# Kernel tuning notes

Measured on AMD Instinct MI355X. Metric: run time of the kernel, lower is better.

The kernel has to match this reference:

```python
import jax, jax.numpy as jnp
import numpy as np

D_MODEL = 2048
N_HEADS = 16
HEAD_DIM = D_MODEL // N_HEADS  # 128
MAX_SEQ = 2048
ROPE_BASE = 10000.0


def _rope(t, start_pos):
    # t: (B, S, Hn, head_dim); standard interleaved-pair RoPE
    B, S, Hn, hd = t.shape
    inv_freq = 1.0 / (ROPE_BASE ** (jnp.arange(0, hd, 2, dtype=jnp.float32) / hd))  # (hd/2,)
    pos = jnp.arange(start_pos, start_pos + S, dtype=jnp.float32)                    # (S,)
    ang = pos[:, None] * inv_freq[None, :]                                           # (S, hd/2)
    cos = jnp.cos(ang)[None, :, None, :]
    sin = jnp.sin(ang)[None, :, None, :]
    x1 = t[..., 0::2]
    x2 = t[..., 1::2]
    o1 = x1 * cos - x2 * sin
    o2 = x1 * sin + x2 * cos
    return jnp.stack([o1, o2], axis=-1).reshape(t.shape)


def setup_inputs() -> dict:
    key = jax.random.key(0)
    ks = jax.random.split(key, 9)
    s = 1.0 / np.sqrt(D_MODEL)
    return {
        "x": jax.random.normal(ks[0], (4, 2048, D_MODEL), dtype=jnp.float32),
        "wq": jax.random.uniform(ks[1], (D_MODEL, D_MODEL), jnp.float32, -s, s),
        "bq": jax.random.uniform(ks[2], (D_MODEL,), jnp.float32, -s, s),
        "wk": jax.random.uniform(ks[3], (D_MODEL, HEAD_DIM), jnp.float32, -s, s),
        "bk": jax.random.uniform(ks[4], (HEAD_DIM,), jnp.float32, -s, s),
        "wv": jax.random.uniform(ks[5], (D_MODEL, HEAD_DIM), jnp.float32, -s, s),
        "bv": jax.random.uniform(ks[6], (HEAD_DIM,), jnp.float32, -s, s),
        "wo": jax.random.uniform(ks[7], (D_MODEL, D_MODEL), jnp.float32, -s, s),
        "bo": jax.random.uniform(ks[8], (D_MODEL,), jnp.float32, -s, s),
    }


def reference(x, wq, bq, wk, bk, wv, bv, wo, bo):
    # Prefill path: start_pos=0, kv_cache=None.
    B, S, D = x.shape
    q = (x @ wq + bq).reshape(B, S, N_HEADS, HEAD_DIM)  # (B,S,H,hd)
    k = (x @ wk + bk).reshape(B, S, 1, HEAD_DIM)        # (B,S,1,hd) shared KV head
    v = (x @ wv + bv).reshape(B, S, 1, HEAD_DIM)
    q = _rope(q, 0)
    k = _rope(k, 0)
    qh = q.transpose(0, 2, 1, 3)          # (B,H,S,hd)
    kh = k.transpose(0, 2, 1, 3)          # (B,1,S,hd)  -> kv_cache entry
    vh = v.transpose(0, 2, 1, 3)
    scores = jnp.einsum("bhqd,bkd->bhqk", qh, kh[:, 0]) / jnp.sqrt(
        jnp.asarray(HEAD_DIM, dtype=x.dtype))
    # original buffer: tril(ones) with zeros replaced by -inf -> allowed positions get +1
    tril = jnp.tril(jnp.ones((S, S), dtype=bool))
    mask = jnp.where(tril, jnp.asarray(1.0, x.dtype), jnp.asarray(-jnp.inf, x.dtype))
    scores = scores + mask[None, None, :, :]
    p = jax.nn.softmax(scores, axis=-1)                 # (B,H,S,S)
    attn = jnp.einsum("bhqk,bkd->bhqd", p, vh[:, 0])    # (B,H,S,hd)
    out = attn.transpose(0, 2, 1, 3).reshape(B, S, D) @ wo + bo
    return (out, kh, vh)
```

## Files before the change

kernel.cpp:

```cpp
#include <hip/hip_runtime.h>
#include <hip/hip_bf16.h>
#include <cstdint>
#include <cstddef>

#define SEQ 2048
#define DM 2048
#define NHEADS 16
#define HD 128
#define NTOK 8192
#define BATCH 4

typedef __bf16 bf16_t;
typedef bf16_t bf16x8 __attribute__((ext_vector_type(8)));
typedef float f32x4 __attribute__((ext_vector_type(4)));

__device__ __forceinline__ void async_copy16(const bf16_t* g, bf16_t* l) {
  __builtin_amdgcn_global_load_lds(
      (const __attribute__((address_space(1))) unsigned int*)g,
      (__attribute__((address_space(3))) unsigned int*)l, 16, 0, 0);
}

__device__ __forceinline__ void store_out(float* p, float v)  { *p = v; }
__device__ __forceinline__ void store_out(bf16_t* p, float v) { *p = (bf16_t)v; }


__global__ void convert_x_bf16(const float* __restrict__ in, bf16_t* __restrict__ out, int n4) {
  int i = blockIdx.x * 256 + threadIdx.x;
  if (i >= n4) return;
  float4 v = ((const float4*)in)[i];
  union { ushort4 u; bf16_t b[4]; } o;
  o.b[0] = (bf16_t)v.x; o.b[1] = (bf16_t)v.y; o.b[2] = (bf16_t)v.z; o.b[3] = (bf16_t)v.w;
  *(ushort4*)(out + (size_t)i * 4) = o.u;
}

__global__ void transpose_f32_to_bf16(const float* __restrict__ in, bf16_t* __restrict__ out,
                                      int R, int C) {
  __shared__ float tile[32][33];
  int c0 = blockIdx.x * 32, r0 = blockIdx.y * 32;
  int tx = threadIdx.x & 31, ty = threadIdx.x >> 5;
  for (int i = ty; i < 32; i += 8) tile[i][tx] = in[(size_t)(r0 + i) * C + c0 + tx];
  __syncthreads();
  for (int i = ty; i < 32; i += 8) out[(size_t)(c0 + i) * R + r0 + tx] = (bf16_t)tile[tx][i];
}

template <typename OutT>
__global__ __launch_bounds__(256) void gemm_bt(const bf16_t* __restrict__ A,
                                               const bf16_t* __restrict__ Bt,
                                               const float* __restrict__ bias,
                                               OutT* __restrict__ C, int M, int N, int K) {
  __shared__ bf16_t As[128 * 32];
  __shared__ bf16_t Bs[128 * 32];
  const int tid = threadIdx.x;
  const int lane = tid & 63;
  const int wv = tid >> 6;
  const int wi = wv >> 1, wj = wv & 1;
  const int quad = lane >> 4, l16 = lane & 15;
  const size_t m0 = (size_t)blockIdx.x * 128, n0 = (size_t)blockIdx.y * 128;

  f32x4 acc[4][4] = {};

  const bf16_t* ag = A + (m0 + (tid >> 2)) * K + (tid & 3) * 8;
  const bf16_t* bg = Bt + (n0 + (tid >> 2)) * K + (tid & 3) * 8;
  bf16_t* asd = As + tid * 8;
  bf16_t* bsd = Bs + tid * 8;
  const int nk = K >> 5;
  for (int kt = 0; kt < nk; kt++) {
    async_copy16(ag, asd);
    async_copy16(ag + (size_t)64 * K, asd + 64 * 32);
    async_copy16(bg, bsd);
    async_copy16(bg + (size_t)64 * K, bsd + 64 * 32);
    ag += 32; bg += 32;
    __syncthreads();
    bf16x8 af[4], bf[4];
#pragma unroll
    for (int mt = 0; mt < 4; mt++)
      af[mt] = *(const bf16x8*)(As + (wi * 64 + mt * 16 + l16) * 32 + quad * 8);
#pragma unroll
    for (int nt = 0; nt < 4; nt++)
      bf[nt] = *(const bf16x8*)(Bs + (wj * 64 + nt * 16 + l16) * 32 + quad * 8);
#pragma unroll
    for (int mt = 0; mt < 4; mt++)
#pragma unroll
      for (int nt = 0; nt < 4; nt++)
        acc[mt][nt] = __builtin_amdgcn_mfma_f32_16x16x32_bf16(af[mt], bf[nt], acc[mt][nt], 0, 0, 0);
    __syncthreads();
  }
#pragma unroll
  for (int nt = 0; nt < 4; nt++) {
    float bb = bias[n0 + wj * 64 + nt * 16 + l16];
#pragma unroll
    for (int mt = 0; mt < 4; mt++) {
      size_t row = m0 + wi * 64 + mt * 16 + quad * 4;
      size_t col = n0 + wj * 64 + nt * 16 + l16;
#pragma unroll
      for (int r = 0; r < 4; r++) store_out(&C[(row + r) * N + col], acc[mt][nt][r] + bb);
    }
  }
}

#define ROPE_C 0.14391156831212787f
#define ATT_SCALE 0.1275174462517703f

__global__ void rope_q_kernel(bf16_t* __restrict__ q) {
  int idx = blockIdx.x * 256 + threadIdx.x;
  int tok = idx >> 8;
  int c0 = (idx & 255) * 8;
  int s = tok & (SEQ - 1);
  int d0 = c0 & (HD - 1);
  union { uint4 u; ushort us[8]; } v;
  v.u = *(const uint4*)(q + (size_t)tok * DM + c0);
  float x[8];
#pragma unroll
  for (int j = 0; j < 8; j++) x[j] = __uint_as_float((uint32_t)v.us[j] << 16);
#pragma unroll
  for (int j = 0; j < 4; j++) {
    int i = (d0 >> 1) + j;
    float fr = __expf(-(float)i * ROPE_C);
    float ang = (float)s * fr;
    float sn, cs; __sincosf(ang, &sn, &cs);
    float o1 = (x[2 * j] * cs - x[2 * j + 1] * sn) * ATT_SCALE;
    float o2 = (x[2 * j] * sn + x[2 * j + 1] * cs) * ATT_SCALE;
    x[2 * j] = o1; x[2 * j + 1] = o2;
  }
  union { uint4 u; ushort us[8]; } w;
#pragma unroll
  for (int j = 0; j < 8; j++) {
    union { float f; uint32_t u; } t; t.f = x[j];
    uint32_t r = (t.u + 0x7fff + ((t.u >> 16) & 1)) >> 16;
    w.us[j] = (ushort)r;
  }
  *(uint4*)(q + (size_t)tok * DM + c0) = w.u;
}

__global__ void rope_kv_kernel(const float* __restrict__ kvf, float* __restrict__ kh,
                               float* __restrict__ vh, bf16_t* __restrict__ kbf) {
  int idx = blockIdx.x * 256 + threadIdx.x;
  int t = idx >> 6;
  int i = idx & 63;
  int s = t & (SEQ - 1);
  const float* base = kvf + (size_t)t * 256;
  float x1 = base[2 * i], x2 = base[2 * i + 1];
  float fr = __expf(-(float)i * ROPE_C);
  float ang = (float)s * fr;
  float sn, cs; __sincosf(ang, &sn, &cs);
  float k1 = x1 * cs - x2 * sn, k2 = x1 * sn + x2 * cs;
  size_t o = (size_t)t * HD + 2 * i;
  kh[o] = k1; kh[o + 1] = k2;
  kbf[o] = (bf16_t)k1; kbf[o + 1] = (bf16_t)k2;
  vh[o] = base[128 + 2 * i];
  vh[o + 1] = base[128 + 2 * i + 1];
}

__global__ void transpose_v_kernel(const float* __restrict__ kvf, bf16_t* __restrict__ vT) {
  __shared__ float tile[32][33];
  int b = blockIdx.z;
  int s0 = blockIdx.x * 32, d0 = blockIdx.y * 32;
  int tx = threadIdx.x & 31, ty = threadIdx.x >> 5;
  for (int i = ty; i < 32; i += 8)
    tile[i][tx] = kvf[(size_t)(b * SEQ + s0 + i) * 256 + 128 + d0 + tx];
  __syncthreads();
  for (int i = ty; i < 32; i += 8)
    vT[(size_t)b * HD * SEQ + (size_t)(d0 + i) * SEQ + s0 + tx] = (bf16_t)tile[tx][i];
}

__global__ __launch_bounds__(256, 2) void flash_attn_kernel(const bf16_t* __restrict__ Q,
                                                            const bf16_t* __restrict__ Kb,
                                                            const bf16_t* __restrict__ VT,
                                                            bf16_t* __restrict__ O) {
  __shared__ bf16_t Ks[2][64 * 128];
  __shared__ bf16_t Vs[2][64 * 128];
  const int tid = threadIdx.x;
  const int lane = tid & 63;
  const int wv = tid >> 6;
  const int quad = lane >> 4, l16 = lane & 15;
  const int pr = blockIdx.x, h = blockIdx.y, b = blockIdx.z;

  const bf16_t* kbase = Kb + (size_t)b * SEQ * HD;
  const bf16_t* vbase = VT + (size_t)b * HD * SEQ;

  int cur = 0;
#pragma unroll
  for (int i = 0; i < 4; i++) {
    int p = i * 256 + tid;
    int kr = p >> 4, kc = (p & 15) ^ (kr & 15);
    async_copy16(kbase + (size_t)kr * HD + kc * 8, &Ks[0][p * 8]);
    int vr = p >> 3, vc = (p & 7) ^ (vr & 7);
    async_copy16(vbase + (size_t)vr * SEQ + vc * 8, &Vs[0][p * 8]);
  }

#pragma unroll 1
  for (int ph = 0; ph < 2; ph++) {
    const int qt = ph ? pr : 15 - pr;
    const int nkt = 2 * qt + 2;

    bf16x8 qf[2][4];
#pragma unroll
    for (int nt = 0; nt < 2; nt++) {
      size_t qrow = (size_t)b * SEQ + qt * 128 + wv * 32 + nt * 16 + l16;
      const bf16_t* qp = Q + qrow * DM + h * HD + quad * 8;
#pragma unroll
      for (int ks = 0; ks < 4; ks++) qf[nt][ks] = *(const bf16x8*)(qp + ks * 32);
    }

    f32x4 oacc[8][2] = {};
    float l2[2] = {0.f, 0.f};

#pragma unroll 1
    for (int kt = 0; kt < nkt; kt++) {
      asm volatile("s_waitcnt lgkmcnt(0)" ::: "memory");
      __builtin_amdgcn_sched_barrier(0);
      __builtin_amdgcn_s_barrier();
      __builtin_amdgcn_sched_barrier(0);

      const int has_next = !(ph == 1 && kt == nkt - 1);
      if (has_next) {
        const int k0n = (kt + 1 < nkt) ? (kt + 1) * 64 : 0;
        bf16_t* kd = &Ks[cur ^ 1][0];
        bf16_t* vd = &Vs[cur ^ 1][0];
#pragma unroll
        for (int i = 0; i < 4; i++) {
          int p = i * 256 + tid;
          int kr = p >> 4, kc = (p & 15) ^ (kr & 15);
          async_copy16(kbase + (size_t)(k0n + kr) * HD + kc * 8, kd + p * 8);
          int vr = p >> 3, vc = (p & 7) ^ (vr & 7);
          async_copy16(vbase + (size_t)vr * SEQ + k0n + vc * 8, vd + p * 8);
        }
        asm volatile("s_waitcnt vmcnt(8)" ::: "memory");
      } else {
        asm volatile("s_waitcnt vmcnt(0)" ::: "memory");
      }
      __builtin_amdgcn_sched_barrier(0);
      __builtin_amdgcn_s_barrier();
      __builtin_amdgcn_sched_barrier(0);

      const bf16_t* KsC = &Ks[cur][0];
      const bf16_t* VsC = &Vs[cur][0];

      f32x4 sa[4][2] = {};
#pragma unroll
      for (int ks = 0; ks < 4; ks++) {
        bf16x8 ak[4];
#pragma unroll
        for (int mt = 0; mt < 4; mt++) {
          int row = mt * 16 + l16;
          int c = (ks * 4 + quad) ^ l16;
          ak[mt] = *(const bf16x8*)(KsC + (row * 16 + c) * 8);
        }
        __builtin_amdgcn_s_setprio(1);
#pragma unroll
        for (int mt = 0; mt < 4; mt++)
#pragma unroll
          for (int nt = 0; nt < 2; nt++)
            sa[mt][nt] = __builtin_amdgcn_mfma_f32_16x16x32_bf16(ak[mt], qf[nt][ks], sa[mt][nt], 0, 0, 0);
        __builtin_amdgcn_s_setprio(0);
      }

      if (kt >= 2 * qt) {
        const int k0c = kt * 64;
#pragma unroll
        for (int mt = 0; mt < 4; mt++)
#pragma unroll
          for (int nt = 0; nt < 2; nt++) {
            int kg0 = k0c + mt * 16 + quad * 4;
            int qg = qt * 128 + wv * 32 + nt * 16 + l16;
#pragma unroll
            for (int r = 0; r < 4; r++)
              if (kg0 + r > qg) sa[mt][nt][r] = -INFINITY;
          }
      }

      bf16x8 bp[2][2];
#pragma unroll
      for (int nt = 0; nt < 2; nt++) {
        float rs = 0.f;
#pragma unroll
        for (int mt = 0; mt < 4; mt++)
#pragma unroll
          for (int r = 0; r < 4; r++) {
            float pv = exp2f(sa[mt][nt][r]);
            sa[mt][nt][r] = pv;
            rs += pv;
          }
        {
          float a0 = rs, a1 = rs;
          asm("v_permlane16_swap_b32 %0, %1" : "+v"(a0), "+v"(a1));
          rs = a0 + a1;
          float c0 = rs, c1 = rs;
          asm("v_permlane32_swap_b32 %0, %1" : "+v"(c0), "+v"(c1));
          rs = c0 + c1;
        }
        l2[nt] += rs;

        uint32_t d0[4], d1[4];
#pragma unroll
        for (int m = 0; m < 4; m++) {
          asm("v_cvt_pk_bf16_f32 %0, %1, %2" : "=v"(d0[m]) : "v"(sa[m][nt][0]), "v"(sa[m][nt][1]));
          asm("v_cvt_pk_bf16_f32 %0, %1, %2" : "=v"(d1[m]) : "v"(sa[m][nt][2]), "v"(sa[m][nt][3]));
        }
#pragma unroll
        for (int ks = 0; ks < 2; ks++) {
          uint32_t w0 = d0[2 * ks], w2 = d0[2 * ks + 1];
          uint32_t w1 = d1[2 * ks], w3 = d1[2 * ks + 1];
          asm("v_permlane32_swap_b32 %0, %1" : "+v"(w0), "+v"(w2));
          asm("v_permlane16_swap_b32 %0, %1" : "+v"(w0), "+v"(w2));
          asm("v_permlane32_swap_b32 %0, %1" : "+v"(w1), "+v"(w3));
          asm("v_permlane16_swap_b32 %0, %1" : "+v"(w1), "+v"(w3));
          union { uint32_t u[4]; bf16x8 v; } pk_;
          pk_.u[0] = w0; pk_.u[1] = w1; pk_.u[2] = w2; pk_.u[3] = w3;
          bp[nt][ks] = pk_.v;
        }
      }

#pragma unroll
      for (int ks = 0; ks < 2; ks++)
#pragma unroll
        for (int dm = 0; dm < 8; dm++) {
          int row = dm * 16 + l16;
          int c = (ks * 4 + quad) ^ (row & 7);
          bf16x8 av = *(const bf16x8*)(VsC + (row * 8 + c) * 8);
          __builtin_amdgcn_s_setprio(1);
#pragma unroll
          for (int nt = 0; nt < 2; nt++)
            oacc[dm][nt] = __builtin_amdgcn_mfma_f32_16x16x32_bf16(av, bp[nt][ks], oacc[dm][nt], 0, 0, 0);
          __builtin_amdgcn_s_setprio(0);
        }

      cur ^= 1;
    }

    float inv[2];
#pragma unroll
    for (int nt = 0; nt < 2; nt++) inv[nt] = 1.f / l2[nt];
#pragma unroll
    for (int dm = 0; dm < 8; dm++)
#pragma unroll
      for (int nt = 0; nt < 2; nt++) {
        size_t row = (size_t)b * SEQ + qt * 128 + wv * 32 + nt * 16 + l16;
        size_t col = (size_t)h * HD + dm * 16 + quad * 4;
        union { ushort4 u; bf16_t bb[4]; } pk;
#pragma unroll
        for (int r = 0; r < 4; r++) pk.bb[r] = (bf16_t)(oacc[dm][nt][r] * inv[nt]);
        *(ushort4*)(O + row * DM + col) = pk.u;
      }
  }
}


extern "C" void kernel_launch(void* const* d_in, const int* in_sizes, int n_in,
                              void* d_out, int out_size, void* d_ws, size_t ws_size,
                              hipStream_t stream) {
  const float* x  = (const float*)d_in[0];
  const float* wq = (const float*)d_in[1];
  const float* bq = (const float*)d_in[2];
  const float* wk = (const float*)d_in[3];
  const float* bk = (const float*)d_in[4];
  const float* wv = (const float*)d_in[5];
  const float* bv = (const float*)d_in[6];
  const float* wo = (const float*)d_in[7];
  const float* bo = (const float*)d_in[8];
  char* ws = (char*)d_ws;

  bf16_t* xbf  = (bf16_t*)(ws);
  bf16_t* qbf  = (bf16_t*)(ws + 33554432ull);
  bf16_t* wqT  = (bf16_t*)(ws + 67108864ull);
  bf16_t* woT  = (bf16_t*)(ws + 75497472ull);
  bf16_t* wkvT = (bf16_t*)(ws + 83886080ull);
  float*  kvf  = (float* )(ws + 84934656ull);
  bf16_t* kbf  = (bf16_t*)(ws + 93323264ull);
  bf16_t* vT   = (bf16_t*)(ws + 95420416ull);
  float*  bkv  = (float* )(ws + 97517568ull);
  bf16_t* attn = xbf;

  float* out = (float*)d_out;
  float* kh  = out + 16777216ull;
  float* vh  = kh + 1048576ull;

  hipMemcpyAsync(bkv,       bk, 128 * sizeof(float), hipMemcpyDeviceToDevice, stream);
  hipMemcpyAsync(bkv + 128, bv, 128 * sizeof(float), hipMemcpyDeviceToDevice, stream);

  convert_x_bf16<<<16384, 256, 0, stream>>>(x, xbf, 4194304);
  transpose_f32_to_bf16<<<dim3(64, 64), 256, 0, stream>>>(wq, wqT, 2048, 2048);
  transpose_f32_to_bf16<<<dim3(64, 64), 256, 0, stream>>>(wo, woT, 2048, 2048);
  transpose_f32_to_bf16<<<dim3(4, 64), 256, 0, stream>>>(wk, wkvT, 2048, 128);
  transpose_f32_to_bf16<<<dim3(4, 64), 256, 0, stream>>>(wv, wkvT + 128 * 2048, 2048, 128);

  gemm_bt<bf16_t><<<dim3(64, 16), 256, 0, stream>>>(xbf, wqT, bq, qbf, 8192, 2048, 2048);
  gemm_bt<float ><<<dim3(64, 2),  256, 0, stream>>>(xbf, wkvT, bkv, kvf, 8192, 256, 2048);

  rope_q_kernel<<<8192, 256, 0, stream>>>(qbf);
  rope_kv_kernel<<<2048, 256, 0, stream>>>(kvf, kh, vh, kbf);
  transpose_v_kernel<<<dim3(64, 4, 4), 256, 0, stream>>>(kvf, vT);

  flash_attn_kernel<<<dim3(8, 16, 4), 256, 0, stream>>>(qbf, kbf, vT, attn);

  gemm_bt<float><<<dim3(64, 16), 256, 0, stream>>>(attn, woT, bo, out, 8192, 2048, 2048);
}
```

Before: 557.9 us.

## Add 256x256-tile pipelined bf16 GEMM for Q and output projections

```diff
diff --git a/kernel.cpp b/kernel.cpp
--- a/kernel.cpp
+++ b/kernel.cpp
@@ -22,6 +22,10 @@
 
 __device__ __forceinline__ void store_out(float* p, float v)  { *p = v; }
 __device__ __forceinline__ void store_out(bf16_t* p, float v) { *p = (bf16_t)v; }
+
+#define SB  __builtin_amdgcn_sched_barrier(0)
+#define BAR __builtin_amdgcn_s_barrier()
+#define LGKM0 asm volatile("s_waitcnt lgkmcnt(0)" ::: "memory")
 
 
 __global__ void convert_x_bf16(const float* __restrict__ in, bf16_t* __restrict__ out, int n4) {
@@ -96,6 +100,133 @@
       for (int r = 0; r < 4; r++) store_out(&C[(row + r) * N + col], acc[mt][nt][r] + bb);
     }
   }
+}
+
+template <typename OutT>
+__global__ __launch_bounds__(512, 2) void gemm256(const bf16_t* __restrict__ A,
+                                                  const bf16_t* __restrict__ Bt,
+                                                  const float* __restrict__ bias,
+                                                  OutT* __restrict__ C, int M, int N, int K) {
+  extern __shared__ char smem_raw[];
+  bf16_t* As_ = (bf16_t*)smem_raw;
+  bf16_t* Bs_ = As_ + 32768;
+
+  const int tid = threadIdx.x;
+  const int lane = tid & 63;
+  const int wv = tid >> 6;
+  const int wr = wv >> 2, wc = wv & 3;
+  const int quad = lane >> 4, l16 = lane & 15;
+
+  const int bid = blockIdx.x;
+  const int g = (bid & 7) * 32 + (bid >> 3);
+  const size_t m0 = (size_t)(g >> 3) * 256;
+  const size_t n0 = (size_t)(g & 7) * 256;
+
+  auto mkrow = [](int s) { int rp = s >> 3; int Cc = (s & 7) ^ (rp & 7); return rp * 2 + (Cc >> 2); };
+  auto mkkc  = [](int s) { int rp = s >> 3; int Cc = (s & 7) ^ (rp & 7); return (Cc & 3) * 8; };
+  const bf16_t* pA0 = A  + (size_t)(m0 + mkrow(tid)) * K + mkkc(tid);
+  const bf16_t* pA1 = A  + (size_t)(m0 + mkrow(tid + 512)) * K + mkkc(tid + 512);
+  const bf16_t* pB0 = Bt + (size_t)(n0 + mkrow(tid)) * K + mkkc(tid);
+  const bf16_t* pB1 = Bt + (size_t)(n0 + mkrow(tid + 512)) * K + mkkc(tid + 512);
+
+#define STAGE_A(SLOT, KH, KT) do { \
+    async_copy16(pA0 + (size_t)(KT) * 64 + (KH) * 32, As_ + (SLOT) * 16384 + (KH) * 8192 + tid * 8); \
+    async_copy16(pA1 + (size_t)(KT) * 64 + (KH) * 32, As_ + (SLOT) * 16384 + (KH) * 8192 + (tid + 512) * 8); \
+  } while (0)
+#define STAGE_B(SLOT, KH, KT) do { \
+    async_copy16(pB0 + (size_t)(KT) * 64 + (KH) * 32, Bs_ + (SLOT) * 16384 + (KH) * 8192 + tid * 8); \
+    async_copy16(pB1 + (size_t)(KT) * 64 + (KH) * 32, Bs_ + (SLOT) * 16384 + (KH) * 8192 + (tid + 512) * 8); \
+  } while (0)
+
+  int aoffs[8], boffs[4];
+#pragma unroll
+  for (int mi = 0; mi < 8; mi++) {
+    int row = wr * 128 + mi * 16 + l16;
+    int rp = row >> 1, Cc = (row & 1) * 4 + quad;
+    aoffs[mi] = rp * 64 + (Cc ^ (rp & 7)) * 8;
+  }
+#pragma unroll
+  for (int ni = 0; ni < 4; ni++) {
+    int row = wc * 64 + ni * 16 + l16;
+    int rp = row >> 1, Cc = (row & 1) * 4 + quad;
+    boffs[ni] = rp * 64 + (Cc ^ (rp & 7)) * 8;
+  }
+
+  f32x4 acc[8][4] = {};
+  bf16x8 afr[8], b0, b1;
+
+#define LOAD_A(SLOT, KS) do { _Pragma("unroll") \
+    for (int mi = 0; mi < 8; mi++) afr[mi] = *(const bf16x8*)(As_ + (SLOT) * 16384 + (KS) * 8192 + aoffs[mi]); \
+  } while (0)
+#define LOAD_B2(SLOT, KS, NF0) do { \
+    b0 = *(const bf16x8*)(Bs_ + (SLOT) * 16384 + (KS) * 8192 + boffs[NF0]); \
+    b1 = *(const bf16x8*)(Bs_ + (SLOT) * 16384 + (KS) * 8192 + boffs[(NF0) + 1]); \
+  } while (0)
+#define MFMA16(NF0) do { __builtin_amdgcn_s_setprio(1); _Pragma("unroll") \
+    for (int mi = 0; mi < 8; mi++) { \
+      acc[mi][NF0] = __builtin_amdgcn_mfma_f32_16x16x32_bf16(afr[mi], b0, acc[mi][NF0], 0, 0, 0); \
+      acc[mi][(NF0) + 1] = __builtin_amdgcn_mfma_f32_16x16x32_bf16(afr[mi], b1, acc[mi][(NF0) + 1], 0, 0, 0); \
+    } __builtin_amdgcn_s_setprio(0); } while (0)
+
+  const int NI = K >> 7;
+
+  STAGE_A(0, 0, 0); STAGE_B(0, 0, 0);
+  STAGE_A(0, 1, 0); STAGE_B(0, 1, 0);
+  STAGE_A(1, 0, 1); STAGE_B(1, 0, 1);
+  asm volatile("s_waitcnt vmcnt(0)" ::: "memory");
+  SB; BAR; SB;
+
+#pragma unroll 1
+  for (int j = 0; j < NI; j++) {
+    const int last = (j == NI - 1);
+    LOAD_A(0, 0); LOAD_B2(0, 0, 0);
+    STAGE_A(1, 1, 2 * j + 1);
+    SB; BAR; LGKM0; SB; MFMA16(0); SB; BAR;
+    LOAD_B2(0, 0, 2);
+    STAGE_B(1, 1, 2 * j + 1);
+    SB; BAR; LGKM0; SB; MFMA16(2); SB; BAR;
+    LOAD_A(0, 1); LOAD_B2(0, 1, 0);
+    if (!last) STAGE_A(0, 0, 2 * j + 2);
+    SB; BAR; LGKM0; SB; MFMA16(0); SB; BAR;
+    LOAD_B2(0, 1, 2);
+    if (!last) STAGE_B(0, 0, 2 * j + 2);
+    SB;
+    if (!last) { asm volatile("s_waitcnt vmcnt(4)" ::: "memory"); }
+    else       { asm volatile("s_waitcnt vmcnt(0)" ::: "memory"); }
+    BAR; LGKM0; SB; MFMA16(2); SB; BAR;
+    LOAD_A(1, 0); LOAD_B2(1, 0, 0);
+    if (!last) STAGE_A(0, 1, 2 * j + 2);
+    SB; BAR; LGKM0; SB; MFMA16(0); SB; BAR;
+    LOAD_B2(1, 0, 2);
+    if (!last) STAGE_B(0, 1, 2 * j + 2);
+    SB; BAR; LGKM0; SB; MFMA16(2); SB; BAR;
+    LOAD_A(1, 1); LOAD_B2(1, 1, 0);
+    if (!last) STAGE_A(1, 0, 2 * j + 3);
+    SB; BAR; LGKM0; SB; MFMA16(0); SB; BAR;
+    LOAD_B2(1, 1, 2);
+    if (!last) STAGE_B(1, 0, 2 * j + 3);
+    SB;
+    if (!last) { asm volatile("s_waitcnt vmcnt(4)" ::: "memory"); }
+    else       { asm volatile("s_waitcnt vmcnt(0)" ::: "memory"); }
+    BAR; LGKM0; SB; MFMA16(2); SB; BAR;
+  }
+
+#pragma unroll
+  for (int ni = 0; ni < 4; ni++) {
+    size_t col = n0 + wc * 64 + ni * 16 + l16;
+    float bb = bias[col];
+#pragma unroll
+    for (int mi = 0; mi < 8; mi++) {
+      size_t row = m0 + wr * 128 + mi * 16 + quad * 4;
+#pragma unroll
+      for (int r = 0; r < 4; r++) store_out(&C[(row + r) * N + col], acc[mi][ni][r] + bb);
+    }
+  }
+#undef STAGE_A
+#undef STAGE_B
+#undef LOAD_A
+#undef LOAD_B2
+#undef MFMA16
 }
 
 #define ROPE_C 0.14391156831212787f
@@ -208,9 +339,7 @@
 #pragma unroll 1
     for (int kt = 0; kt < nkt; kt++) {
       asm volatile("s_waitcnt lgkmcnt(0)" ::: "memory");
-      __builtin_amdgcn_sched_barrier(0);
-      __builtin_amdgcn_s_barrier();
-      __builtin_amdgcn_sched_barrier(0);
+      SB; BAR; SB;
 
       const int has_next = !(ph == 1 && kt == nkt - 1);
       if (has_next) {
@@ -229,9 +358,7 @@
       } else {
         asm volatile("s_waitcnt vmcnt(0)" ::: "memory");
       }
-      __builtin_amdgcn_sched_barrier(0);
-      __builtin_amdgcn_s_barrier();
-      __builtin_amdgcn_sched_barrier(0);
+      SB; BAR; SB;
 
       const bf16_t* KsC = &Ks[cur][0];
       const bf16_t* VsC = &Vs[cur][0];
@@ -375,6 +502,9 @@
   float* kh  = out + 16777216ull;
   float* vh  = kh + 1048576ull;
 
+  hipFuncSetAttribute((const void*)gemm256<bf16_t>, hipFuncAttributeMaxDynamicSharedMemorySize, 131072);
+  hipFuncSetAttribute((const void*)gemm256<float>,  hipFuncAttributeMaxDynamicSharedMemorySize, 131072);
+
   hipMemcpyAsync(bkv,       bk, 128 * sizeof(float), hipMemcpyDeviceToDevice, stream);
   hipMemcpyAsync(bkv + 128, bv, 128 * sizeof(float), hipMemcpyDeviceToDevice, stream);
 
@@ -384,8 +514,8 @@
   transpose_f32_to_bf16<<<dim3(4, 64), 256, 0, stream>>>(wk, wkvT, 2048, 128);
   transpose_f32_to_bf16<<<dim3(4, 64), 256, 0, stream>>>(wv, wkvT + 128 * 2048, 2048, 128);
 
-  gemm_bt<bf16_t><<<dim3(64, 16), 256, 0, stream>>>(xbf, wqT, bq, qbf, 8192, 2048, 2048);
-  gemm_bt<float ><<<dim3(64, 2),  256, 0, stream>>>(xbf, wkvT, bkv, kvf, 8192, 256, 2048);
+  gemm256<bf16_t><<<256, 512, 131072, stream>>>(xbf, wqT, bq, qbf, 8192, 2048, 2048);
+  gemm_bt<float ><<<dim3(64, 2), 256, 0, stream>>>(xbf, wkvT, bkv, kvf, 8192, 256, 2048);
 
   rope_q_kernel<<<8192, 256, 0, stream>>>(qbf);
   rope_kv_kernel<<<2048, 256, 0, stream>>>(kvf, kh, vh, kbf);
@@ -393,5 +523,5 @@
 
   flash_attn_kernel<<<dim3(8, 16, 4), 256, 0, stream>>>(qbf, kbf, vT, attn);
 
-  gemm_bt<float><<<dim3(64, 16), 256, 0, stream>>>(attn, woT, bo, out, 8192, 2048, 2048);
-}
+  gemm256<float><<<256, 512, 131072, stream>>>(attn, woT, bo, out, 8192, 2048, 2048);
+}
```

Result: faster. 485.4 us (-13.0%).
